# Kernel tuning notes

Measured on AMD Instinct MI355X. Metric: run time of the kernel, lower is better.

## Reference

```python
import jax, jax.numpy as jnp
import numpy as np

IN_F = 4096
OUT_F = 4096
Q_RANK = 2
R_RANK = 2
SCALE = 1.0
B, S = 2, 2048


def setup_inputs() -> dict:
    key = jax.random.key(0)
    ks = jax.random.split(key, 8)
    inp = jax.random.normal(ks[0], (B, S, IN_F), jnp.float32)
    # Q, R come from a QR decomposition of linear.weight.t(); random stand-ins with
    # matching shapes and O(1) scale are fine for a numerical baseline.
    Q = jax.random.normal(ks[1], (IN_F, OUT_F), jnp.float32) / np.sqrt(IN_F).astype(np.float32)
    R = jax.random.normal(ks[2], (OUT_F, OUT_F), jnp.float32) / np.sqrt(OUT_F).astype(np.float32)
    # kron_Q1/Q2 are initialized to identity in __init__ (never re-initialized);
    # add small noise so the rotation path is non-trivial.
    sq1 = IN_F // Q_RANK
    kron_Q1 = jnp.eye(sq1, dtype=jnp.float32) + 0.01 * jax.random.normal(ks[3], (sq1, sq1), jnp.float32)
    kron_Q2 = jnp.eye(Q_RANK, dtype=jnp.float32) + 0.01 * jax.random.normal(ks[4], (Q_RANK, Q_RANK), jnp.float32)
    # kron_R1/R2 use normal init with std = 1/size.
    sr1 = OUT_F // R_RANK
    kron_R1 = jax.random.normal(ks[5], (sr1, sr1), jnp.float32) / sr1
    kron_R2 = jax.random.normal(ks[6], (R_RANK, R_RANK), jnp.float32) / R_RANK
    # lambda_matrix inits to zeros; use small noise so the delta term is exercised.
    lambda_matrix = 0.01 * jax.random.normal(ks[7], (OUT_F,), jnp.float32)
    return {"input": inp, "Q": Q, "R": R, "kron_Q1": kron_Q1, "kron_Q2": kron_Q2,
            "kron_R1": kron_R1, "kron_R2": kron_R2, "lambda_matrix": lambda_matrix}


def reference(input, Q, R, kron_Q1, kron_Q2, kron_R1, kron_R2, lambda_matrix):
    rotation = jnp.kron(kron_Q1, kron_Q2)          # [in, in]
    orth = jnp.kron(kron_R1, kron_R2)              # [out, out]
    # orth @ diag(lambda) @ orth.T without materializing diag
    R_eff = R + (orth * lambda_matrix[None, :]) @ orth.T  # [out, out]
    W_t = rotation @ (Q @ R_eff)                   # [in, out]
    # F.linear(input, W_t.t()) == input @ W_t; dropout is identity in eval; bias=False
    return (input @ W_t) * SCALE
```

## Files before the change

### kernel.cpp

```cpp
#include <hip/hip_runtime.h>
#include <stdint.h>


typedef unsigned short u16;
typedef short bf16x8 __attribute__((ext_vector_type(8)));
typedef float f32x4 __attribute__((ext_vector_type(4)));

__device__ __forceinline__ u16 f2bf(float f) {
  union { float f; uint32_t u; } v; v.f = f;
  return (u16)((v.u + 0x7FFFu + ((v.u >> 16) & 1u)) >> 16);
}

__device__ __forceinline__ void store_out(float* p, float v) { *p = v; }
__device__ __forceinline__ void store_out(u16* p, float v) { *p = f2bf(v); }

__device__ __forceinline__ void gload_lds16(const u16* g, u16* l) {
  __builtin_amdgcn_global_load_lds(
      (__attribute__((address_space(1))) void*)(uintptr_t)g,
      (__attribute__((address_space(3))) void*)l, 16, 0, 0);
}

#define MFMA16(a, b, c) __builtin_amdgcn_mfma_f32_16x16x32_bf16((a), (b), (c), 0, 0, 0)

template <typename OutT>
__global__ __launch_bounds__(512, 2) void gemm256(
    const u16* __restrict__ A, const u16* __restrict__ Bt, OutT* __restrict__ C,
    int M, int N, int K, int ldC, long long sA, long long sC) {
  extern __shared__ __align__(16) u16 smem[];
  u16* ldsA = smem;
  u16* ldsB = smem + 32768;

  const int tid  = (int)threadIdx.x;
  const int lane = tid & 63;
  const int wid  = tid >> 6;
  const int wr   = wid >> 2;
  const int wc   = wid & 3;

  const int tilesX = (int)gridDim.x;
  const int tilesXY = tilesX * (int)gridDim.y;
  const int nwg = tilesXY * (int)gridDim.z;
  const int bid = ((int)blockIdx.z * (int)gridDim.y + (int)blockIdx.y) * tilesX + (int)blockIdx.x;
  const int swz = (bid & 7) * (nwg >> 3) + (bid >> 3);
  const int z   = swz / tilesXY;
  const int rem = swz % tilesXY;
  const int brow = (rem / tilesX) << 8;
  const int bcol = (rem % tilesX) << 8;
  A += (size_t)z * sA;
  C += (size_t)z * sC;

  const int lr = lane & 15, lg = lane >> 4, h = lr >> 1;
  const int sf = (lg + ((lr & 1) << 2)) ^ h;
  const int abase = wr * 4096 + h * 64 + sf * 8;
  const int bbase = (wc >> 1) * 4096 + (wc & 1) * 2048 + h * 64 + sf * 8;

  const int kp   = (tid & 7) ^ ((tid >> 3) & 7);
  const int srow = 2 * (tid >> 3) + (kp >> 2);
  const int scol = (kp & 3) << 3;
  const size_t gA0 = (size_t)(brow + srow) * K + scol;
  const size_t gB0 = (size_t)(bcol + srow) * K + scol;
  const size_t rstep = (size_t)K << 7;
  const int sdst = wid * 512;

  const int NC = K >> 5;

  f32x4 acc[8][4] = {};
  bf16x8 af[8], bf[4];

#define STG_A(c, rh) gload_lds16(A + gA0 + (rh) * rstep + (size_t)(c) * 32, \
    ldsA + ((c) & 3) * 8192 + (rh) * 4096 + sdst)
#define STG_B(c, rh) gload_lds16(Bt + gB0 + (rh) * rstep + (size_t)(c) * 32, \
    ldsB + ((c) & 3) * 8192 + (rh) * 4096 + sdst)
#define VM8 asm volatile("s_waitcnt vmcnt(8)" ::: "memory")
#define VM4 asm volatile("s_waitcnt vmcnt(4)" ::: "memory")
#define VM0 asm volatile("s_waitcnt vmcnt(0)" ::: "memory")
#define NOPW (void)0

#define P_EVEN(bb, S, W) do {                                                   \
    const u16* _pa = ldsA + (bb) * 8192 + abase;                                \
    const u16* _pb = ldsB + (bb) * 8192 + bbase;                                \
    _Pragma("unroll")                                                           \
    for (int m = 0; m < 4; ++m) af[m] = *(const bf16x8*)(_pa + m * 512);        \
    _Pragma("unroll")                                                           \
    for (int n = 0; n < 4; ++n) bf[n] = *(const bf16x8*)(_pb + n * 512);        \
    S;                                                                          \
    __builtin_amdgcn_s_barrier();                                               \
    asm volatile("s_waitcnt lgkmcnt(0)" ::: "memory");                          \
    __builtin_amdgcn_sched_barrier(0);                                          \
    __builtin_amdgcn_s_setprio(1);                                              \
    _Pragma("unroll")                                                           \
    for (int m = 0; m < 4; ++m)                                                 \
      _Pragma("unroll")                                                         \
      for (int n = 0; n < 4; ++n)                                               \
        acc[m][n] = MFMA16(af[m], bf[n], acc[m][n]);                            \
    __builtin_amdgcn_s_setprio(0);                                              \
    W;                                                                          \
    __builtin_amdgcn_sched_barrier(0);                                          \
    __builtin_amdgcn_s_barrier();                                               \
  } while (0)

#define P_ODD(bb, S, W) do {                                                    \
    const u16* _pa = ldsA + (bb) * 8192 + abase;                                \
    _Pragma("unroll")                                                           \
    for (int m = 0; m < 4; ++m) af[4 + m] = *(const bf16x8*)(_pa + (4 + m) * 512); \
    S;                                                                          \
    __builtin_amdgcn_s_barrier();                                               \
    asm volatile("s_waitcnt lgkmcnt(0)" ::: "memory");                          \
    __builtin_amdgcn_sched_barrier(0);                                          \
    __builtin_amdgcn_s_setprio(1);                                              \
    _Pragma("unroll")                                                           \
    for (int m = 0; m < 4; ++m)                                                 \
      _Pragma("unroll")                                                         \
      for (int n = 0; n < 4; ++n)                                               \
        acc[4 + m][n] = MFMA16(af[4 + m], bf[n], acc[4 + m][n]);                \
    __builtin_amdgcn_s_setprio(0);                                              \
    W;                                                                          \
    __builtin_amdgcn_sched_barrier(0);                                          \
    __builtin_amdgcn_s_barrier();                                               \
  } while (0)

#define ITER(bb, c, DO3, DO4, W1, W3) do {                                      \
    P_EVEN((bb),     if (DO3) { STG_A((c) + 3, 0); STG_A((c) + 3, 1); }, NOPW); \
    P_ODD ((bb),     if (DO3) { STG_B((c) + 3, 0); STG_B((c) + 3, 1); }, W1);   \
    P_EVEN((bb) + 1, if (DO4) { STG_A((c) + 4, 0); STG_A((c) + 4, 1); }, NOPW); \
    P_ODD ((bb) + 1, if (DO4) { STG_B((c) + 4, 0); STG_B((c) + 4, 1); }, W3);   \
  } while (0)

  STG_A(0, 0); STG_A(0, 1); STG_B(0, 0); STG_B(0, 1);
  STG_A(1, 0); STG_A(1, 1); STG_B(1, 0); STG_B(1, 1);
  STG_A(2, 0); STG_A(2, 1); STG_B(2, 0); STG_B(2, 1);
  VM8;
  __builtin_amdgcn_sched_barrier(0);
  __builtin_amdgcn_s_barrier();

  for (int c = 0; c + 4 < NC; c += 4) {
    ITER(0, c,     1, 1, VM8, VM8);
    ITER(2, c + 2, 1, 1, VM8, VM8);
  }
  ITER(0, NC - 4, 1, 0, VM8, VM4);
  ITER(2, NC - 2, 0, 0, VM0, NOPW);

#undef ITER
#undef P_EVEN
#undef P_ODD
#undef STG_A
#undef STG_B
#undef VM8
#undef VM4
#undef VM0
#undef NOPW

#pragma unroll
  for (int m = 0; m < 8; ++m) {
    const int r0 = brow + wr * 128 + m * 16 + lg * 4;
#pragma unroll
    for (int n = 0; n < 4; ++n) {
      const int cc = bcol + wc * 64 + n * 16 + lr;
#pragma unroll
      for (int j = 0; j < 4; ++j)
        store_out(&C[(size_t)(r0 + j) * ldC + cc], acc[m][n][j]);
    }
  }
}

__global__ void trans_kernel(const float* __restrict__ in, u16* __restrict__ out, int n) {
  __shared__ float t[32][33];
  const int bx = (int)blockIdx.x * 32, by = (int)blockIdx.y * 32;
  const int x = (int)threadIdx.x, y0 = (int)threadIdx.y;
#pragma unroll
  for (int dy = 0; dy < 32; dy += 8)
    t[y0 + dy][x] = in[(size_t)(bx + y0 + dy) * n + by + x];
  __syncthreads();
#pragma unroll
  for (int dy = 0; dy < 32; dy += 8)
    out[(size_t)(by + y0 + dy) * n + bx + x] = f2bf(t[x][y0 + dy]);
}

__global__ void transperm_kernel(const float* __restrict__ in, u16* __restrict__ out) {
  __shared__ float t[32][33];
  const int bx = (int)blockIdx.x * 32, by = (int)blockIdx.y * 32;
  const int x = (int)threadIdx.x, y0 = (int)threadIdx.y;
#pragma unroll
  for (int dy = 0; dy < 32; dy += 8)
    t[y0 + dy][x] = in[(size_t)(bx + y0 + dy) * 4096 + by + x];
  __syncthreads();
  const int r = bx + x;
  const int cp = ((r & 1) << 11) | (r >> 1);
#pragma unroll
  for (int dy = 0; dy < 32; dy += 8)
    out[(size_t)(by + y0 + dy) * 4096 + cp] = f2bf(t[x][y0 + dy]);
}

__global__ void transadd_kernel(const float* __restrict__ R, const float* __restrict__ Dsub,
                                u16* __restrict__ out) {
  __shared__ float t[32][33];
  const int bx = (int)blockIdx.x * 32, by = (int)blockIdx.y * 32;
  const int x = (int)threadIdx.x, y0 = (int)threadIdx.y;
#pragma unroll
  for (int dy = 0; dy < 32; dy += 8)
    t[y0 + dy][x] = R[(size_t)(bx + y0 + dy) * 4096 + by + x];
  __syncthreads();
  const int j = bx + x;
#pragma unroll
  for (int dy = 0; dy < 32; dy += 8) {
    const int i = by + y0 + dy;
    const int s = ((i & 1) << 1) | (j & 1);
    const float d = Dsub[(size_t)s * 4194304 + ((size_t)(i >> 1) << 11) + (j >> 1)];
    out[(size_t)i * 4096 + j] = f2bf(t[x][y0 + dy] + d);
  }
}

__global__ void scale_r1_kernel(const float* __restrict__ R1, const float* __restrict__ R2,
                                const float* __restrict__ lam,
                                u16* __restrict__ R1bf, u16* __restrict__ Asc) {
  const int idx = (int)blockIdx.x * 256 + (int)threadIdx.x;
  const int i1 = idx >> 9, k1 = (idx & 511) << 2;
  const float4 r1 = *(const float4*)(R1 + (size_t)i1 * 2048 + k1);
  const float4 l0 = *(const float4*)(lam + 2 * k1);
  const float4 l1 = *(const float4*)(lam + 2 * k1 + 4);
  const float le[4] = {l0.x, l0.z, l1.x, l1.z};
  const float lo[4] = {l0.y, l0.w, l1.y, l1.w};
  const float rv[4] = {r1.x, r1.y, r1.z, r1.w};
  ushort4 rb;
  rb.x = f2bf(r1.x); rb.y = f2bf(r1.y); rb.z = f2bf(r1.z); rb.w = f2bf(r1.w);
  *(ushort4*)(R1bf + (size_t)i1 * 2048 + k1) = rb;
#pragma unroll
  for (int s = 0; s < 4; ++s) {
    const int i2 = s >> 1, j2 = s & 1;
    const float c0 = R2[i2 * 2] * R2[j2 * 2];
    const float c1 = R2[i2 * 2 + 1] * R2[j2 * 2 + 1];
    ushort4 o;
    u16* dst = Asc + (size_t)s * 4194304 + (size_t)i1 * 2048 + k1;
    o.x = f2bf(rv[0] * (le[0] * c0 + lo[0] * c1));
    o.y = f2bf(rv[1] * (le[1] * c0 + lo[1] * c1));
    o.z = f2bf(rv[2] * (le[2] * c0 + lo[2] * c1));
    o.w = f2bf(rv[3] * (le[3] * c0 + lo[3] * c1));
    *(ushort4*)dst = o;
  }
}

__global__ void tprep_kernel(const float* __restrict__ in, const float* __restrict__ Q2,
                             u16* __restrict__ T) {
  const int idx = (int)blockIdx.x * 256 + (int)threadIdx.x;
  const int s = idx >> 9, k1 = (idx & 511) << 2;
  const float4 a = *(const float4*)(in + (size_t)s * 4096 + 2 * k1);
  const float4 b = *(const float4*)(in + (size_t)s * 4096 + 2 * k1 + 4);
  const float e[4] = {a.x, a.z, b.x, b.z};
  const float o[4] = {a.y, a.w, b.y, b.w};
  const float q00 = Q2[0], q01 = Q2[1], q10 = Q2[2], q11 = Q2[3];
  ushort4 t0, t1;
  t0.x = f2bf(e[0] * q00 + o[0] * q10); t1.x = f2bf(e[0] * q01 + o[0] * q11);
  t0.y = f2bf(e[1] * q00 + o[1] * q10); t1.y = f2bf(e[1] * q01 + o[1] * q11);
  t0.z = f2bf(e[2] * q00 + o[2] * q10); t1.z = f2bf(e[2] * q01 + o[2] * q11);
  t0.w = f2bf(e[3] * q00 + o[3] * q10); t1.w = f2bf(e[3] * q01 + o[3] * q11);
  *(ushort4*)(T + (size_t)s * 2048 + k1) = t0;
  *(ushort4*)(T + 8388608 + (size_t)s * 2048 + k1) = t1;
}

extern "C" void kernel_launch(void* const* d_in, const int* in_sizes, int n_in,
                              void* d_out, int out_size, void* d_ws, size_t ws_size,
                              hipStream_t stream) {
  const float* input = (const float*)d_in[0];
  const float* Q     = (const float*)d_in[1];
  const float* R     = (const float*)d_in[2];
  const float* Q1    = (const float*)d_in[3];
  const float* Q2    = (const float*)d_in[4];
  const float* R1    = (const float*)d_in[5];
  const float* R2    = (const float*)d_in[6];
  const float* lam   = (const float*)d_in[7];
  float* out = (float*)d_out;

  const size_t MB = 1024ull * 1024ull;
  char* ws = (char*)d_ws;
  u16* R1bf  = (u16*)(ws + 0 * MB);
  u16* Asc   = (u16*)(ws + 8 * MB);
  u16* Q1tb  = (u16*)(ws + 40 * MB);
  u16* T     = (u16*)(ws + 48 * MB);
  u16* Qtp   = (u16*)(ws + 80 * MB);
  u16* rteff = (u16*)(ws + 112 * MB);
  u16* X1p   = (u16*)(ws + 144 * MB);
  u16* X2    = Asc;
  float* Dsub = (float*)d_out;

  {
    void (*pf)(const u16*, const u16*, float*, int, int, int, int, long long, long long) = gemm256<float>;
    void (*pb)(const u16*, const u16*, u16*, int, int, int, int, long long, long long)   = gemm256<u16>;
    (void)hipFuncSetAttribute((const void*)pf, hipFuncAttributeMaxDynamicSharedMemorySize, 131072);
    (void)hipFuncSetAttribute((const void*)pb, hipFuncAttributeMaxDynamicSharedMemorySize, 131072);
  }

  const dim3 tb(32, 8);
  trans_kernel<<<dim3(64, 64), tb, 0, stream>>>(Q1, Q1tb, 2048);
  transperm_kernel<<<dim3(128, 128), tb, 0, stream>>>(Q, Qtp);
  scale_r1_kernel<<<4096, 256, 0, stream>>>(R1, R2, lam, R1bf, Asc);
  tprep_kernel<<<8192, 256, 0, stream>>>(input, Q2, T);
  gemm256<float><<<dim3(8, 8, 4), 512, 131072, stream>>>(
      Asc, R1bf, Dsub, 2048, 2048, 2048, 2048, 4194304LL, 4194304LL);
  transadd_kernel<<<dim3(128, 128), tb, 0, stream>>>(R, Dsub, rteff);
  gemm256<u16><<<dim3(8, 16, 2), 512, 131072, stream>>>(
      T, Q1tb, X1p, 4096, 2048, 2048, 4096, 8388608LL, 2048LL);
  gemm256<u16><<<dim3(16, 16, 1), 512, 131072, stream>>>(
      X1p, Qtp, X2, 4096, 4096, 4096, 4096, 0LL, 0LL);
  gemm256<float><<<dim3(16, 16, 1), 512, 131072, stream>>>(
      X2, rteff, out, 4096, 4096, 4096, 4096, 0LL, 0LL);
}
```

Measured before the change: 478.2 us.

## Switch GEMM inner loop from 16x16x32 to 32x32x16 bf16 MFMA

```diff
diff --git a/kernel.cpp b/kernel.cpp
--- a/kernel.cpp
+++ b/kernel.cpp
@@ -4,7 +4,7 @@
 
 typedef unsigned short u16;
 typedef short bf16x8 __attribute__((ext_vector_type(8)));
-typedef float f32x4 __attribute__((ext_vector_type(4)));
+typedef float f32x16 __attribute__((ext_vector_type(16)));
 
 __device__ __forceinline__ u16 f2bf(float f) {
   union { float f; uint32_t u; } v; v.f = f;
@@ -20,7 +20,7 @@
       (__attribute__((address_space(3))) void*)l, 16, 0, 0);
 }
 
-#define MFMA16(a, b, c) __builtin_amdgcn_mfma_f32_16x16x32_bf16((a), (b), (c), 0, 0, 0)
+#define MFMA32(a, b, c) __builtin_amdgcn_mfma_f32_32x32x16_bf16((a), (b), (c), 0, 0, 0)
 
 template <typename OutT>
 __global__ __launch_bounds__(512, 2) void gemm256(
@@ -48,10 +48,14 @@
   A += (size_t)z * sA;
   C += (size_t)z * sC;
 
-  const int lr = lane & 15, lg = lane >> 4, h = lr >> 1;
-  const int sf = (lg + ((lr & 1) << 2)) ^ h;
-  const int abase = wr * 4096 + h * 64 + sf * 8;
-  const int bbase = (wc >> 1) * 4096 + (wc & 1) * 2048 + h * 64 + sf * 8;
+  const int l31 = lane & 31;
+  const int lg2 = lane >> 5;
+  const int h32 = l31 >> 1;
+  const int par = lane & 1;
+  const int sfa0 = (((lg2 + 4 * par) ^ (h32 & 7)) << 3);
+  const int sfa1 = (((2 + lg2 + 4 * par) ^ (h32 & 7)) << 3);
+  const int abase = wr * 4096 + h32 * 64;
+  const int bbase = (wc >> 1) * 4096 + (wc & 1) * 2048 + h32 * 64;
 
   const int kp   = (tid & 7) ^ ((tid >> 3) & 7);
   const int srow = 2 * (tid >> 3) + (kp >> 2);
@@ -63,8 +67,8 @@
 
   const int NC = K >> 5;
 
-  f32x4 acc[8][4] = {};
-  bf16x8 af[8], bf[4];
+  f32x16 acc[4][2] = {};
+  bf16x8 af[2][2], bf[2][2];
 
 #define STG_A(c, rh) gload_lds16(A + gA0 + (rh) * rstep + (size_t)(c) * 32, \
     ldsA + ((c) & 3) * 8192 + (rh) * 4096 + sdst)
@@ -78,43 +82,49 @@
 #define P_EVEN(bb, S, W) do {                                                   \
     const u16* _pa = ldsA + (bb) * 8192 + abase;                                \
     const u16* _pb = ldsB + (bb) * 8192 + bbase;                                \
-    _Pragma("unroll")                                                           \
-    for (int m = 0; m < 4; ++m) af[m] = *(const bf16x8*)(_pa + m * 512);        \
-    _Pragma("unroll")                                                           \
-    for (int n = 0; n < 4; ++n) bf[n] = *(const bf16x8*)(_pb + n * 512);        \
+    af[0][0] = *(const bf16x8*)(_pa + sfa0);                                    \
+    bf[0][0] = *(const bf16x8*)(_pb + sfa0);                                    \
+    af[0][1] = *(const bf16x8*)(_pa + sfa1);                                    \
+    bf[0][1] = *(const bf16x8*)(_pb + sfa1);                                    \
+    af[1][0] = *(const bf16x8*)(_pa + 1024 + sfa0);                             \
+    bf[1][0] = *(const bf16x8*)(_pb + 1024 + sfa0);                             \
+    af[1][1] = *(const bf16x8*)(_pa + 1024 + sfa1);                             \
+    bf[1][1] = *(const bf16x8*)(_pb + 1024 + sfa1);                             \
     S;                                                                          \
     __builtin_amdgcn_s_barrier();                                               \
-    asm volatile("s_waitcnt lgkmcnt(0)" ::: "memory");                          \
-    __builtin_amdgcn_sched_barrier(0);                                          \
     __builtin_amdgcn_s_setprio(1);                                              \
-    _Pragma("unroll")                                                           \
-    for (int m = 0; m < 4; ++m)                                                 \
-      _Pragma("unroll")                                                         \
-      for (int n = 0; n < 4; ++n)                                               \
-        acc[m][n] = MFMA16(af[m], bf[n], acc[m][n]);                            \
+    acc[0][0] = MFMA32(af[0][0], bf[0][0], acc[0][0]);                          \
+    acc[0][0] = MFMA32(af[0][1], bf[0][1], acc[0][0]);                          \
+    acc[0][1] = MFMA32(af[0][0], bf[1][0], acc[0][1]);                          \
+    acc[0][1] = MFMA32(af[0][1], bf[1][1], acc[0][1]);                          \
+    acc[1][0] = MFMA32(af[1][0], bf[0][0], acc[1][0]);                          \
+    acc[1][0] = MFMA32(af[1][1], bf[0][1], acc[1][0]);                          \
+    acc[1][1] = MFMA32(af[1][0], bf[1][0], acc[1][1]);                          \
+    acc[1][1] = MFMA32(af[1][1], bf[1][1], acc[1][1]);                          \
     __builtin_amdgcn_s_setprio(0);                                              \
     W;                                                                          \
-    __builtin_amdgcn_sched_barrier(0);                                          \
     __builtin_amdgcn_s_barrier();                                               \
   } while (0)
 
 #define P_ODD(bb, S, W) do {                                                    \
     const u16* _pa = ldsA + (bb) * 8192 + abase;                                \
-    _Pragma("unroll")                                                           \
-    for (int m = 0; m < 4; ++m) af[4 + m] = *(const bf16x8*)(_pa + (4 + m) * 512); \
+    af[0][0] = *(const bf16x8*)(_pa + 2048 + sfa0);                             \
+    af[0][1] = *(const bf16x8*)(_pa + 2048 + sfa1);                             \
+    af[1][0] = *(const bf16x8*)(_pa + 3072 + sfa0);                             \
+    af[1][1] = *(const bf16x8*)(_pa + 3072 + sfa1);                             \
     S;                                                                          \
     __builtin_amdgcn_s_barrier();                                               \
-    asm volatile("s_waitcnt lgkmcnt(0)" ::: "memory");                          \
-    __builtin_amdgcn_sched_barrier(0);                                          \
     __builtin_amdgcn_s_setprio(1);                                              \
-    _Pragma("unroll")                                                           \
-    for (int m = 0; m < 4; ++m)                                                 \
-      _Pragma("unroll")                                                         \
-      for (int n = 0; n < 4; ++n)                                               \
-        acc[4 + m][n] = MFMA16(af[4 + m], bf[n], acc[4 + m][n]);                \
+    acc[2][0] = MFMA32(af[0][0], bf[0][0], acc[2][0]);                          \
+    acc[2][0] = MFMA32(af[0][1], bf[0][1], acc[2][0]);                          \
+    acc[2][1] = MFMA32(af[0][0], bf[1][0], acc[2][1]);                          \
+    acc[2][1] = MFMA32(af[0][1], bf[1][1], acc[2][1]);                          \
+    acc[3][0] = MFMA32(af[1][0], bf[0][0], acc[3][0]);                          \
+    acc[3][0] = MFMA32(af[1][1], bf[0][1], acc[3][0]);                          \
+    acc[3][1] = MFMA32(af[1][0], bf[1][0], acc[3][1]);                          \
+    acc[3][1] = MFMA32(af[1][1], bf[1][1], acc[3][1]);                          \
     __builtin_amdgcn_s_setprio(0);                                              \
     W;                                                                          \
-    __builtin_amdgcn_sched_barrier(0);                                          \
     __builtin_amdgcn_s_barrier();                                               \
   } while (0)
 
@@ -129,7 +139,6 @@
   STG_A(1, 0); STG_A(1, 1); STG_B(1, 0); STG_B(1, 1);
   STG_A(2, 0); STG_A(2, 1); STG_B(2, 0); STG_B(2, 1);
   VM8;
-  __builtin_amdgcn_sched_barrier(0);
   __builtin_amdgcn_s_barrier();
 
   for (int c = 0; c + 4 < NC; c += 4) {
@@ -150,14 +159,16 @@
 #undef NOPW
 
 #pragma unroll
-  for (int m = 0; m < 8; ++m) {
-    const int r0 = brow + wr * 128 + m * 16 + lg * 4;
-#pragma unroll
-    for (int n = 0; n < 4; ++n) {
-      const int cc = bcol + wc * 64 + n * 16 + lr;
-#pragma unroll
-      for (int j = 0; j < 4; ++j)
-        store_out(&C[(size_t)(r0 + j) * ldC + cc], acc[m][n][j]);
+  for (int m = 0; m < 4; ++m) {
+    const int rb = brow + wr * 128 + m * 32 + 4 * lg2;
+#pragma unroll
+    for (int n = 0; n < 2; ++n) {
+      const int cc = bcol + wc * 64 + n * 32 + l31;
+#pragma unroll
+      for (int q = 0; q < 4; ++q)
+#pragma unroll
+        for (int j = 0; j < 4; ++j)
+          store_out(&C[(size_t)(rb + 8 * q + j) * ldC + cc], acc[m][n][q * 4 + j]);
     }
   }
 }
```

After: 516.7 us. 1.08x slower.
